# Kernel optimization log

Hardware: AMD Instinct MI355X
Metric: run time of the kernel (lower is better)

## Reference

```python
import jax, jax.numpy as jnp
import numpy as np

B, C, T = 64, 64, 1000   # batch, EEG channels (input_dim), timesteps
H = 512                   # hidden_dim
L = 3                     # num_layers
NC = 5                    # num_classes


def setup_inputs() -> dict:
    key = jax.random.key(0)
    ks = jax.random.split(key, 9)
    s_in = 1.0 / np.sqrt(H)  # torch LSTM init scale
    x = jax.random.normal(ks[0], (B, C, T), dtype=jnp.float32)
    W_ih0 = jax.random.uniform(ks[1], (4 * H, C), jnp.float32, -s_in, s_in)
    W_ih_rest = jax.random.uniform(ks[2], (L - 1, 4 * H, H), jnp.float32, -s_in, s_in)
    W_hh = jax.random.uniform(ks[3], (L, 4 * H, H), jnp.float32, -s_in, s_in)
    b_ih = jax.random.uniform(ks[4], (L, 4 * H), jnp.float32, -s_in, s_in)
    b_hh = jax.random.uniform(ks[5], (L, 4 * H), jnp.float32, -s_in, s_in)
    W_fc = jax.random.uniform(ks[6], (NC, H), jnp.float32, -s_in, s_in)
    b_fc = jax.random.uniform(ks[7], (NC,), jnp.float32, -s_in, s_in)
    return {"x": x, "W_ih0": W_ih0, "W_ih_rest": W_ih_rest, "W_hh": W_hh,
            "b_ih": b_ih, "b_hh": b_hh, "W_fc": W_fc, "b_fc": b_fc}


def _lstm_layer(x_tbc, W_ih, W_hh, b):
    """x_tbc: [T, B, in]. Returns (h_seq [T,B,H], h_T [B,H]). Gate order i,f,g,o (PyTorch)."""
    # Precompute input projections for all timesteps: [T, B, 4H]
    xg = jnp.einsum('tbi,gi->tbg', x_tbc, W_ih) + b

    def step(carry, xg_t):
        h, c = carry
        gates = xg_t + h @ W_hh.T  # [B, 4H]
        i, f, g, o = jnp.split(gates, 4, axis=-1)
        i, f, o = jax.nn.sigmoid(i), jax.nn.sigmoid(f), jax.nn.sigmoid(o)
        g = jnp.tanh(g)
        c = f * c + i * g
        h = o * jnp.tanh(c)
        return (h, c), h

    Bn = x_tbc.shape[1]
    h0 = jnp.zeros((Bn, H), x_tbc.dtype)
    (hT, _), h_seq = jax.lax.scan(step, (h0, h0), xg)
    return h_seq, hT


def reference(x, W_ih0, W_ih_rest, W_hh, b_ih, b_hh, W_fc, b_fc):
    # input_type='signal': [B, C, T] -> batch_first [B, T, C]; scan over time-major [T, B, C]
    seq = jnp.transpose(x, (2, 0, 1))  # [T, B, C]
    hT = None
    for l in range(L):
        W_ih = W_ih0 if l == 0 else W_ih_rest[l - 1]
        seq, hT = _lstm_layer(seq, W_ih, W_hh[l], b_ih[l] + b_hh[l])
    # dropout=0 (inference): identity
    return hT @ W_fc.T + b_fc  # [B, NC]
```

## Files before the change

kernel.cpp:

```cpp
#include <hip/hip_runtime.h>
#include <cstdint>

#define TB 64
#define TC 64
#define TT 1000
#define TH 512
#define NCLS 5
#define NTHR 512
#define STEPS 1002

#define H0_OFF 0
#define H1_OFF 8192
#define H2_OFF 16384
#define X_OFF  24576
#define SC_OFF 32768
#define SC_W   864
#define LDS_FLOATS (SC_OFF + 8 * SC_W)
#define LDS_BYTES  (LDS_FLOATS * 4)

__device__ __forceinline__ float sigf(float x) { return 1.0f / (1.0f + expf(-x)); }


__device__ __forceinline__ void group_barrier(int* gb, int s, unsigned xcc,
                                              int occ_mine, int nxcd) {
  __syncthreads();
  if (threadIdx.x == 0) {
    const int t = s + 1;
    int a = __hip_atomic_fetch_add(gb + 16 + xcc, 1, __ATOMIC_RELAXED, __HIP_MEMORY_SCOPE_AGENT);
    if (a == occ_mine * t - 1) {
      __threadfence();
      __hip_atomic_fetch_add(gb + 32, 1, __ATOMIC_RELAXED, __HIP_MEMORY_SCOPE_AGENT);
    }
    while (__hip_atomic_load(gb + 32, __ATOMIC_RELAXED, __HIP_MEMORY_SCOPE_AGENT) < nxcd * t)
      __builtin_amdgcn_s_sleep(1);
  }
  __syncthreads();
}

__device__ __forceinline__ void dot4(float& acc, const float4 a, const float4 b) {
  acc = fmaf(a.x, b.x, acc); acc = fmaf(a.y, b.y, acc);
  acc = fmaf(a.z, b.z, acc); acc = fmaf(a.w, b.w, acc);
}

__device__ __forceinline__ void gload_lds16_cg(const char* gsrc_lane, char* lds_base) {
  __builtin_amdgcn_global_load_lds(
      (const __attribute__((address_space(1))) unsigned int*)gsrc_lane,
      (__attribute__((address_space(3))) unsigned int*)lds_base, 16, 0, 0x11);
}

__global__ __launch_bounds__(NTHR) __attribute__((amdgpu_waves_per_eu(2, 2)))
void lstm_pipe(
    const float* __restrict__ x, const float* __restrict__ Wih0,
    const float* __restrict__ WihR, const float* __restrict__ Whh,
    const float* __restrict__ bih, const float* __restrict__ bhh,
    float* __restrict__ hbuf, int* __restrict__ bar)
{
  __shared__ float lds[LDS_FLOATS];
  const int tid = threadIdx.x;
  const int blk = blockIdx.x;
  const int grp = blk >> 6, slot = blk & 63;
  const int b_base = grp * 16;
  const int kk = tid >> 5;
  const int rt = tid & 31;
  const int g  = rt & 3;
  const int cl = rt >> 2;
  const int cell = slot * 8 + cl;
  const int row  = g * TH + cell;
  const int wv = tid >> 6;
  const int lane = tid & 63;

  int* gb = bar + grp * 64;

  float4 wx, wh0[8], w1a[8], w1b[8], w2a[8], w2b[8];
  wx = *(const float4*)(Wih0 + (size_t)row * TC + 4 * kk);
  {
    const float* p0 = Whh  + (size_t)row * TH + 32 * kk;
    const float* p1 = WihR + (size_t)row * TH + 32 * kk;
    const float* p2 = Whh  + (size_t)(2048 + row) * TH + 32 * kk;
    const float* p3 = WihR + (size_t)(2048 + row) * TH + 32 * kk;
    const float* p4 = Whh  + (size_t)(4096 + row) * TH + 32 * kk;
#pragma unroll
    for (int i = 0; i < 8; ++i) {
      wh0[i] = *(const float4*)(p0 + 4 * i);
      w1a[i] = *(const float4*)(p1 + 4 * i);
      w1b[i] = *(const float4*)(p2 + 4 * i);
      w2a[i] = *(const float4*)(p3 + 4 * i);
      w2b[i] = *(const float4*)(p4 + 4 * i);
    }
  }

  const int rl = tid >> 6;
  const int rc = (tid & 63) >> 3;
  const int rb = tid & 7;
  const int rcell = slot * 8 + rc;
  float4 bias_r = make_float4(0.f, 0.f, 0.f, 0.f);
  if (tid < 192) {
    bias_r.x = bih[rl * 2048 + rcell]        + bhh[rl * 2048 + rcell];
    bias_r.y = bih[rl * 2048 +  512 + rcell] + bhh[rl * 2048 +  512 + rcell];
    bias_r.z = bih[rl * 2048 + 1024 + rcell] + bhh[rl * 2048 + 1024 + rcell];
    bias_r.w = bih[rl * 2048 + 1536 + rcell] + bhh[rl * 2048 + 1536 + rcell];
  }
  float cst0 = 0.f, cst1 = 0.f;

  unsigned xcc = 0;
  int occ_mine = 0, nxcd = 0;
  if (tid == 0) {
    unsigned xr;
    asm volatile("s_getreg_b32 %0, hwreg(HW_REG_XCC_ID)" : "=s"(xr));
    xcc = xr & 7;
    __hip_atomic_fetch_add(gb + 8 + xcc, 1, __ATOMIC_RELAXED, __HIP_MEMORY_SCOPE_AGENT);
    int a = __hip_atomic_fetch_add(gb + 0, 1, __ATOMIC_RELAXED, __HIP_MEMORY_SCOPE_AGENT);
    if (a == 63)
      __hip_atomic_fetch_add(gb + 4, 1, __ATOMIC_RELAXED, __HIP_MEMORY_SCOPE_AGENT);
    while (__hip_atomic_load(gb + 4, __ATOMIC_RELAXED, __HIP_MEMORY_SCOPE_AGENT) < 1)
      __builtin_amdgcn_s_sleep(1);
#pragma unroll
    for (int i = 0; i < 8; ++i) {
      int o = __hip_atomic_load(gb + 8 + i, __ATOMIC_RELAXED, __HIP_MEMORY_SCOPE_AGENT);
      if (i == (int)xcc) occ_mine = o;
      if (o > 0) ++nxcd;
    }
  }
  __syncthreads();

  for (int s = 0; s < STEPS; ++s) {
    {
      const bool v0 = (s >= 1 && s <= 1000);
      const bool v1 = (s >= 2);
      const bool v2 = (s >= 3);
      const bool vc = ((s & 7) == 0 && s <= 999);
      if (v0) {
        const char* gp = (const char*)(hbuf + ((size_t)(0 + ((s - 1) & 1)) * TB + b_base) * TH);
        char* lb = (char*)lds + H0_OFF * 4;
#pragma unroll
        for (int i = 0; i < 4; ++i) {
          int off = wv * 4096 + i * 1024;
          gload_lds16_cg(gp + off + lane * 16, lb + off);
        }
      }
      if (v1) {
        const char* gp = (const char*)(hbuf + ((size_t)(2 + ((s - 2) & 1)) * TB + b_base) * TH);
        char* lb = (char*)lds + H1_OFF * 4;
#pragma unroll
        for (int i = 0; i < 4; ++i) {
          int off = wv * 4096 + i * 1024;
          gload_lds16_cg(gp + off + lane * 16, lb + off);
        }
      }
      if (v2) {
        const char* gp = (const char*)(hbuf + ((size_t)(4 + ((s - 3) & 1)) * TB + b_base) * TH);
        char* lb = (char*)lds + H2_OFF * 4;
#pragma unroll
        for (int i = 0; i < 4; ++i) {
          int off = wv * 4096 + i * 1024;
          gload_lds16_cg(gp + off + lane * 16, lb + off);
        }
      }
      if (vc) {
        const int e0 = tid, e1 = tid + NTHR;
        const float* q0 = x + (size_t)(b_base + (e0 >> 6)) * (TC * TT) + (size_t)(e0 & 63) * TT + s;
        const float* q1 = x + (size_t)(b_base + (e1 >> 6)) * (TC * TT) + (size_t)(e1 & 63) * TT + s;
        float4 xa0 = *(const float4*)(q0), xa1 = *(const float4*)(q0 + 4);
        float4 xb0 = *(const float4*)(q1), xb1 = *(const float4*)(q1 + 4);
        float* d0 = lds + X_OFF + (e0 >> 6) * 64 + (e0 & 63);
        float* d1 = lds + X_OFF + (e1 >> 6) * 64 + (e1 & 63);
        d0[0 * 1024] = xa0.x; d0[1 * 1024] = xa0.y; d0[2 * 1024] = xa0.z; d0[3 * 1024] = xa0.w;
        d0[4 * 1024] = xa1.x; d0[5 * 1024] = xa1.y; d0[6 * 1024] = xa1.z; d0[7 * 1024] = xa1.w;
        d1[0 * 1024] = xb0.x; d1[1 * 1024] = xb0.y; d1[2 * 1024] = xb0.z; d1[3 * 1024] = xb0.w;
        d1[4 * 1024] = xb1.x; d1[5 * 1024] = xb1.y; d1[6 * 1024] = xb1.z; d1[7 * 1024] = xb1.w;
      }
    }
    __syncthreads();

#pragma unroll
    for (int p = 0; p < 2; ++p) {
      float a0[8], a1[8], a2[8];
#pragma unroll
      for (int b = 0; b < 8; ++b) { a0[b] = 0.f; a1[b] = 0.f; a2[b] = 0.f; }
#pragma unroll
      for (int b = 0; b < 8; ++b) {
        const int bb = p * 8 + b;
        if (s <= 999) {
          float4 xf = *(const float4*)(lds + X_OFF + (s & 7) * 1024 + bb * 64 + 4 * kk);
          dot4(a0[b], wx, xf);
        }
        if (s >= 1 && s <= 1000) {
          const float* hb = lds + H0_OFF + bb * TH + 32 * kk;
#pragma unroll
          for (int c4 = 0; c4 < 2; ++c4) {
            float4 f0 = *(const float4*)(hb + 16 * c4 + 0);
            float4 f1 = *(const float4*)(hb + 16 * c4 + 4);
            float4 f2 = *(const float4*)(hb + 16 * c4 + 8);
            float4 f3 = *(const float4*)(hb + 16 * c4 + 12);
            if (s <= 999) {
              dot4(a0[b], wh0[4 * c4 + 0], f0); dot4(a0[b], wh0[4 * c4 + 1], f1);
              dot4(a0[b], wh0[4 * c4 + 2], f2); dot4(a0[b], wh0[4 * c4 + 3], f3);
            }
            dot4(a1[b], w1a[4 * c4 + 0], f0); dot4(a1[b], w1a[4 * c4 + 1], f1);
            dot4(a1[b], w1a[4 * c4 + 2], f2); dot4(a1[b], w1a[4 * c4 + 3], f3);
          }
        }
        if (s >= 2) {
          const float* hb = lds + H1_OFF + bb * TH + 32 * kk;
#pragma unroll
          for (int c4 = 0; c4 < 2; ++c4) {
            float4 f0 = *(const float4*)(hb + 16 * c4 + 0);
            float4 f1 = *(const float4*)(hb + 16 * c4 + 4);
            float4 f2 = *(const float4*)(hb + 16 * c4 + 8);
            float4 f3 = *(const float4*)(hb + 16 * c4 + 12);
            if (s <= 1000) {
              dot4(a1[b], w1b[4 * c4 + 0], f0); dot4(a1[b], w1b[4 * c4 + 1], f1);
              dot4(a1[b], w1b[4 * c4 + 2], f2); dot4(a1[b], w1b[4 * c4 + 3], f3);
            }
            dot4(a2[b], w2a[4 * c4 + 0], f0); dot4(a2[b], w2a[4 * c4 + 1], f1);
            dot4(a2[b], w2a[4 * c4 + 2], f2); dot4(a2[b], w2a[4 * c4 + 3], f3);
          }
        }
        if (s >= 3) {
          const float* hb = lds + H2_OFF + bb * TH + 32 * kk;
#pragma unroll
          for (int c4 = 0; c4 < 2; ++c4) {
            float4 f0 = *(const float4*)(hb + 16 * c4 + 0);
            float4 f1 = *(const float4*)(hb + 16 * c4 + 4);
            float4 f2 = *(const float4*)(hb + 16 * c4 + 8);
            float4 f3 = *(const float4*)(hb + 16 * c4 + 12);
            dot4(a2[b], w2b[4 * c4 + 0], f0); dot4(a2[b], w2b[4 * c4 + 1], f1);
            dot4(a2[b], w2b[4 * c4 + 2], f2); dot4(a2[b], w2b[4 * c4 + 3], f3);
          }
        }
      }
#pragma unroll
      for (int b = 0; b < 8; ++b) {
        a0[b] += __shfl_xor(a0[b], 32, 64);
        a1[b] += __shfl_xor(a1[b], 32, 64);
        a2[b] += __shfl_xor(a2[b], 32, 64);
      }
      if ((tid & 32) == 0) {
        float* sb = lds + SC_OFF + wv * SC_W + cl * 36 + g;
#pragma unroll
        for (int b = 0; b < 8; ++b) {
          sb[4 * b]       = a0[b];
          sb[288 + 4 * b] = a1[b];
          sb[576 + 4 * b] = a2[b];
        }
      }
      __syncthreads();
      if (tid < 192) {
        const int tl = s - rl;
        if (tl >= 0 && tl < TT) {
          float sx = 0.f, sy = 0.f, sz = 0.f, sw = 0.f;
          const float* sb = lds + SC_OFF + rl * 288 + rc * 36 + 4 * rb;
#pragma unroll
          for (int w8 = 0; w8 < 8; ++w8) {
            float4 v = *(const float4*)(sb + w8 * SC_W);
            sx += v.x; sy += v.y; sz += v.z; sw += v.w;
          }
          float ii = sigf(sx + bias_r.x);
          float ff = sigf(sy + bias_r.y);
          float gg = tanhf(sz + bias_r.z);
          float oo = sigf(sw + bias_r.w);
          float cprev = p ? cst1 : cst0;
          float cc = (tl == 0) ? ii * gg : fmaf(ff, cprev, ii * gg);
          if (p) cst1 = cc; else cst0 = cc;
          float hh = oo * tanhf(cc);
          hbuf[((size_t)(rl * 2 + (tl & 1)) * TB + b_base + p * 8 + rb) * TH + rcell] = hh;
        }
      }
      if (p == 0) __syncthreads();
    }
    group_barrier(gb, s, xcc, occ_mine, nxcd);
  }
}

__global__ void fc_kernel(const float* __restrict__ hbuf, const float* __restrict__ Wfc,
                          const float* __restrict__ bfc, float* __restrict__ out) {
  int bb = blockIdx.x, lane = threadIdx.x;
  const float* h = hbuf + ((size_t)5 * TB + bb) * TH;
  for (int n = 0; n < NCLS; ++n) {
    float s = 0.f;
    for (int k = lane; k < TH; k += 64) s = fmaf(h[k], Wfc[n * TH + k], s);
    for (int off = 32; off > 0; off >>= 1) s += __shfl_down(s, off, 64);
    if (lane == 0) out[bb * NCLS + n] = s + bfc[n];
  }
}

extern "C" void kernel_launch(void* const* d_in, const int* in_sizes, int n_in,
                              void* d_out, int out_size, void* d_ws, size_t ws_size,
                              hipStream_t stream) {
  const float* x    = (const float*)d_in[0];
  const float* Wih0 = (const float*)d_in[1];
  const float* WihR = (const float*)d_in[2];
  const float* Whh  = (const float*)d_in[3];
  const float* bih  = (const float*)d_in[4];
  const float* bhh  = (const float*)d_in[5];
  const float* Wfc  = (const float*)d_in[6];
  const float* bfc  = (const float*)d_in[7];
  float* out = (float*)d_out;

  char* ws = (char*)d_ws;
  int*   bar  = (int*)ws;
  float* hbuf = (float*)(ws + 1024);

  hipMemsetAsync(bar, 0, 1024, stream);
  lstm_pipe<<<256, NTHR, 0, stream>>>(x, Wih0, WihR, Whh, bih, bhh, hbuf, bar);
  fc_kernel<<<TB, 64, 0, stream>>>(hbuf, Wfc, bfc, out);
}
```

Before: 16.50 ms.

## Split batch into eight groups of eight to double block count

The batch is now split into 8 groups of 8 samples instead of 4 groups of 16, so the persistent pipeline runs 512 blocks instead of 256. Each block makes a single pass over 8 batch rows per step instead of two passes, which drops one reduction/activation phase and its __syncthreads, and shrinks LDS. The x input is loaded every step with one scalar per thread instead of staged 8 steps at a time. The waves_per_eu hint is removed so that two blocks can share a CU. This needs all 512 blocks co-resident for the spin barrier, and each step now does less work per block with the same per-step grid-barrier cost.

Result: slower. 20.02 ms (+21.4%).

```diff
diff --git a/kernel.cpp b/kernel.cpp
--- a/kernel.cpp
+++ b/kernel.cpp
@@ -7,13 +7,16 @@
 #define TH 512
 #define NCLS 5
 #define NTHR 512
+#define BG 8
+#define NGRP 8
+#define NBLK 512
 #define STEPS 1002
 
 #define H0_OFF 0
-#define H1_OFF 8192
-#define H2_OFF 16384
-#define X_OFF  24576
-#define SC_OFF 32768
+#define H1_OFF 4096
+#define H2_OFF 8192
+#define X_OFF  12288
+#define SC_OFF 12800
 #define SC_W   864
 #define LDS_FLOATS (SC_OFF + 8 * SC_W)
 #define LDS_BYTES  (LDS_FLOATS * 4)
@@ -48,7 +51,7 @@
       (__attribute__((address_space(3))) unsigned int*)lds_base, 16, 0, 0x11);
 }
 
-__global__ __launch_bounds__(NTHR) __attribute__((amdgpu_waves_per_eu(2, 2)))
+__global__ __launch_bounds__(NTHR)
 void lstm_pipe(
     const float* __restrict__ x, const float* __restrict__ Wih0,
     const float* __restrict__ WihR, const float* __restrict__ Whh,
@@ -59,7 +62,7 @@
   const int tid = threadIdx.x;
   const int blk = blockIdx.x;
   const int grp = blk >> 6, slot = blk & 63;
-  const int b_base = grp * 16;
+  const int b_base = grp * BG;
   const int kk = tid >> 5;
   const int rt = tid & 31;
   const int g  = rt & 3;
@@ -100,7 +103,7 @@
     bias_r.z = bih[rl * 2048 + 1024 + rcell] + bhh[rl * 2048 + 1024 + rcell];
     bias_r.w = bih[rl * 2048 + 1536 + rcell] + bhh[rl * 2048 + 1536 + rcell];
   }
-  float cst0 = 0.f, cst1 = 0.f;
+  float cst = 0.f;
 
   unsigned xcc = 0;
   int occ_mine = 0, nxcd = 0;
@@ -128,13 +131,12 @@
       const bool v0 = (s >= 1 && s <= 1000);
       const bool v1 = (s >= 2);
       const bool v2 = (s >= 3);
-      const bool vc = ((s & 7) == 0 && s <= 999);
       if (v0) {
         const char* gp = (const char*)(hbuf + ((size_t)(0 + ((s - 1) & 1)) * TB + b_base) * TH);
         char* lb = (char*)lds + H0_OFF * 4;
 #pragma unroll
-        for (int i = 0; i < 4; ++i) {
-          int off = wv * 4096 + i * 1024;
+        for (int i = 0; i < 2; ++i) {
+          int off = wv * 2048 + i * 1024;
           gload_lds16_cg(gp + off + lane * 16, lb + off);
         }
       }
@@ -142,8 +144,8 @@
         const char* gp = (const char*)(hbuf + ((size_t)(2 + ((s - 2) & 1)) * TB + b_base) * TH);
         char* lb = (char*)lds + H1_OFF * 4;
 #pragma unroll
-        for (int i = 0; i < 4; ++i) {
-          int off = wv * 4096 + i * 1024;
+        for (int i = 0; i < 2; ++i) {
+          int off = wv * 2048 + i * 1024;
           gload_lds16_cg(gp + off + lane * 16, lb + off);
         }
       }
@@ -151,41 +153,29 @@
         const char* gp = (const char*)(hbuf + ((size_t)(4 + ((s - 3) & 1)) * TB + b_base) * TH);
         char* lb = (char*)lds + H2_OFF * 4;
 #pragma unroll
-        for (int i = 0; i < 4; ++i) {
-          int off = wv * 4096 + i * 1024;
+        for (int i = 0; i < 2; ++i) {
+          int off = wv * 2048 + i * 1024;
           gload_lds16_cg(gp + off + lane * 16, lb + off);
         }
       }
-      if (vc) {
-        const int e0 = tid, e1 = tid + NTHR;
-        const float* q0 = x + (size_t)(b_base + (e0 >> 6)) * (TC * TT) + (size_t)(e0 & 63) * TT + s;
-        const float* q1 = x + (size_t)(b_base + (e1 >> 6)) * (TC * TT) + (size_t)(e1 & 63) * TT + s;
-        float4 xa0 = *(const float4*)(q0), xa1 = *(const float4*)(q0 + 4);
-        float4 xb0 = *(const float4*)(q1), xb1 = *(const float4*)(q1 + 4);
-        float* d0 = lds + X_OFF + (e0 >> 6) * 64 + (e0 & 63);
-        float* d1 = lds + X_OFF + (e1 >> 6) * 64 + (e1 & 63);
-        d0[0 * 1024] = xa0.x; d0[1 * 1024] = xa0.y; d0[2 * 1024] = xa0.z; d0[3 * 1024] = xa0.w;
-        d0[4 * 1024] = xa1.x; d0[5 * 1024] = xa1.y; d0[6 * 1024] = xa1.z; d0[7 * 1024] = xa1.w;
-        d1[0 * 1024] = xb0.x; d1[1 * 1024] = xb0.y; d1[2 * 1024] = xb0.z; d1[3 * 1024] = xb0.w;
-        d1[4 * 1024] = xb1.x; d1[5 * 1024] = xb1.y; d1[6 * 1024] = xb1.z; d1[7 * 1024] = xb1.w;
+      if (s <= 999) {
+        lds[X_OFF + tid] = x[(size_t)(b_base + (tid >> 6)) * (TC * TT) + (size_t)(tid & 63) * TT + s];
       }
     }
     __syncthreads();
 
-#pragma unroll
-    for (int p = 0; p < 2; ++p) {
+    {
       float a0[8], a1[8], a2[8];
 #pragma unroll
       for (int b = 0; b < 8; ++b) { a0[b] = 0.f; a1[b] = 0.f; a2[b] = 0.f; }
 #pragma unroll
       for (int b = 0; b < 8; ++b) {
-        const int bb = p * 8 + b;
         if (s <= 999) {
-          float4 xf = *(const float4*)(lds + X_OFF + (s & 7) * 1024 + bb * 64 + 4 * kk);
+          float4 xf = *(const float4*)(lds + X_OFF + b * TC + 4 * kk);
           dot4(a0[b], wx, xf);
         }
         if (s >= 1 && s <= 1000) {
-          const float* hb = lds + H0_OFF + bb * TH + 32 * kk;
+          const float* hb = lds + H0_OFF + b * TH + 32 * kk;
 #pragma unroll
           for (int c4 = 0; c4 < 2; ++c4) {
             float4 f0 = *(const float4*)(hb + 16 * c4 + 0);
@@ -201,7 +191,7 @@
           }
         }
         if (s >= 2) {
-          const float* hb = lds + H1_OFF + bb * TH + 32 * kk;
+          const float* hb = lds + H1_OFF + b * TH + 32 * kk;
 #pragma unroll
           for (int c4 = 0; c4 < 2; ++c4) {
             float4 f0 = *(const float4*)(hb + 16 * c4 + 0);
@@ -217,7 +207,7 @@
           }
         }
         if (s >= 3) {
-          const float* hb = lds + H2_OFF + bb * TH + 32 * kk;
+          const float* hb = lds + H2_OFF + b * TH + 32 * kk;
 #pragma unroll
           for (int c4 = 0; c4 < 2; ++c4) {
             float4 f0 = *(const float4*)(hb + 16 * c4 + 0);
@@ -244,29 +234,28 @@
           sb[576 + 4 * b] = a2[b];
         }
       }
-      __syncthreads();
-      if (tid < 192) {
-        const int tl = s - rl;
-        if (tl >= 0 && tl < TT) {
-          float sx = 0.f, sy = 0.f, sz = 0.f, sw = 0.f;
-          const float* sb = lds + SC_OFF + rl * 288 + rc * 36 + 4 * rb;
-#pragma unroll
-          for (int w8 = 0; w8 < 8; ++w8) {
-            float4 v = *(const float4*)(sb + w8 * SC_W);
-            sx += v.x; sy += v.y; sz += v.z; sw += v.w;
-          }
-          float ii = sigf(sx + bias_r.x);
-          float ff = sigf(sy + bias_r.y);
-          float gg = tanhf(sz + bias_r.z);
-          float oo = sigf(sw + bias_r.w);
-          float cprev = p ? cst1 : cst0;
-          float cc = (tl == 0) ? ii * gg : fmaf(ff, cprev, ii * gg);
-          if (p) cst1 = cc; else cst0 = cc;
-          float hh = oo * tanhf(cc);
-          hbuf[((size_t)(rl * 2 + (tl & 1)) * TB + b_base + p * 8 + rb) * TH + rcell] = hh;
-        }
-      }
-      if (p == 0) __syncthreads();
+    }
+    __syncthreads();
+
+    if (tid < 192) {
+      const int tl = s - rl;
+      if (tl >= 0 && tl < TT) {
+        float sx = 0.f, sy = 0.f, sz = 0.f, sw = 0.f;
+        const float* sbr = lds + SC_OFF + rl * 288 + rc * 36 + 4 * rb;
+#pragma unroll
+        for (int w8 = 0; w8 < 8; ++w8) {
+          float4 v = *(const float4*)(sbr + w8 * SC_W);
+          sx += v.x; sy += v.y; sz += v.z; sw += v.w;
+        }
+        float ii = sigf(sx + bias_r.x);
+        float ff = sigf(sy + bias_r.y);
+        float gg = tanhf(sz + bias_r.z);
+        float oo = sigf(sw + bias_r.w);
+        float cc = (tl == 0) ? ii * gg : fmaf(ff, cst, ii * gg);
+        cst = cc;
+        float hh = oo * tanhf(cc);
+        hbuf[((size_t)(rl * 2 + (tl & 1)) * TB + b_base + rb) * TH + rcell] = hh;
+      }
     }
     group_barrier(gb, s, xcc, occ_mine, nxcd);
   }
@@ -299,9 +288,9 @@
 
   char* ws = (char*)d_ws;
   int*   bar  = (int*)ws;
-  float* hbuf = (float*)(ws + 1024);
-
-  hipMemsetAsync(bar, 0, 1024, stream);
-  lstm_pipe<<<256, NTHR, 0, stream>>>(x, Wih0, WihR, Whh, bih, bhh, hbuf, bar);
+  float* hbuf = (float*)(ws + 2048);
+
+  hipMemsetAsync(bar, 0, 2048, stream);
+  lstm_pipe<<<NBLK, NTHR, 0, stream>>>(x, Wih0, WihR, Whh, bih, bhh, hbuf, bar);
   fc_kernel<<<TB, 64, 0, stream>>>(hbuf, Wfc, bfc, out);
 }
```
